# Kernel tuning notes

Hardware: AMD Instinct MI355X
Metric: run time of the kernel (lower is better)

The kernel has to match this reference:

```python
import jax, jax.numpy as jnp
import numpy as np

L_MAX = 3
N = 16384
K = 128
N_ITERS = 2
DEG = [2 * l + 1 for l in range(L_MAX + 1)]  # [1,3,5,7]


def _cg_mask():
    # zero outside selection-rule-valid (l1,l2,l) triangles and valid m ranges
    m = np.zeros((4, 4, 4, 7, 7, 7), np.float32)
    for l1 in range(L_MAX + 1):
        for l2 in range(L_MAX + 1):
            for l in range(L_MAX + 1):
                if abs(l1 - l2) <= l <= l1 + l2:
                    m[l1, l2, l, : 2 * l1 + 1, : 2 * l2 + 1, : 2 * l + 1] = 1.0
    return m


def setup_inputs() -> dict:
    key = jax.random.key(0)
    ks = jax.random.split(key, 8)
    feats = {
        f"f{l}": jax.random.normal(ks[l], (N, DEG[l], K), dtype=jnp.float32)
        for l in range(L_MAX + 1)
    }
    mixer_w = jax.random.normal(ks[4], (N_ITERS + 1, L_MAX + 1, K, K), dtype=jnp.float32) / np.sqrt(K)
    iter_w = jax.random.normal(ks[5], (N_ITERS, L_MAX + 1, K, K), dtype=jnp.float32) / np.sqrt(K)
    cg = jax.random.normal(ks[6], (4, 4, 4, 7, 7, 7), dtype=jnp.float32) * jnp.asarray(_cg_mask())
    return {**feats, "mixer_w": mixer_w, "iter_w": iter_w, "cg": cg}


def _linear(feats, w):
    # per-l channel mixing (bias-free, equivariance-preserving)
    return [jnp.einsum("nmk,kq->nmq", f, w[l]) for l, f in enumerate(feats)]


def _tensor_product(a, b, cg):
    # CG tensor product: out_l[n,m,k] = sum_{l1,l2 valid} sum_{m1,m2} cg[m1,m2,m] a_l1[n,m1,k] b_l2[n,m2,k]
    out = []
    n = a[0].shape[0]
    for l in range(L_MAX + 1):
        acc = jnp.zeros((n, DEG[l], K), dtype=a[0].dtype)
        for l1 in range(L_MAX + 1):
            for l2 in range(L_MAX + 1):
                if abs(l1 - l2) <= l <= l1 + l2:
                    c = cg[l1, l2, l, : DEG[l1], : DEG[l2], : DEG[l]]
                    acc = acc + jnp.einsum("ijm,nik,njk->nmk", c, a[l1], b[l2])
        out.append(acc)
    return out


def reference(f0, f1, f2, f3, mixer_w, iter_w, cg):
    density = [f0, f1, f2, f3]
    mixed = [_linear(density, mixer_w[i]) for i in range(N_ITERS + 1)]
    current = mixed[0]
    for t in range(N_ITERS):
        # CGIteration: tensor_product -> linear -> residual add
        tp = _tensor_product(current, mixed[t + 1], cg)
        tp = _linear(tp, iter_w[t])
        current = [c + p for c, p in zip(current, tp)]
    return tuple(current)
```

## Files before the change

kernel.cpp:

```cpp
#include <hip/hip_runtime.h>
#include <stdint.h>


#define N_ROWS 16384
#define NK (16384 * 128)

typedef float f32x4 __attribute__((ext_vector_type(4)));
typedef short short8 __attribute__((ext_vector_type(8)));
typedef __bf16 bf16x8 __attribute__((ext_vector_type(8)));

__device__ __forceinline__ uint16_t f2b(float f) {
  uint32_t u = __builtin_bit_cast(uint32_t, f);
  u += 0x7FFFu + ((u >> 16) & 1u);
  return (uint16_t)(u >> 16);
}
__device__ __forceinline__ float b2f(uint16_t h) {
  uint32_t u = ((uint32_t)h) << 16;
  return __builtin_bit_cast(float, u);
}
__device__ __forceinline__ f32x4 mfma_bf16(short8 a, short8 b, f32x4 c) {
  return __builtin_amdgcn_mfma_f32_16x16x32_bf16(
      __builtin_bit_cast(bf16x8, a), __builtin_bit_cast(bf16x8, b), c, 0, 0, 0);
}

__device__ __forceinline__ void tile_decode(int T, int& l, int& row0) {
  l = (T >= 1024) + (T >= 4096) + (T >= 9216);
  row0 = (T - l * l * 1024) * 16;
}
__device__ __forceinline__ int l_of_m(int m) { return (m > 0) + (m > 3) + (m > 8); }

__global__ __launch_bounds__(256) void k0_prep(
    const float* __restrict__ mixw, const float* __restrict__ iterw,
    const float* __restrict__ cg,
    uint16_t* __restrict__ wtmix, uint16_t* __restrict__ wtiter,
    uint16_t* __restrict__ ccat) {
  int idx = blockIdx.x * 256 + threadIdx.x;
  const int NMIX = 3 * 4 * 16384, NITR = 2 * 4 * 16384;
  if (idx < NMIX) {
    int il = idx >> 14, rem = idx & 16383, q = rem >> 7, k = rem & 127;
    wtmix[idx] = f2b(mixw[il * 16384 + k * 128 + q]);
  } else if (idx < NMIX + NITR) {
    int o = idx - NMIX;
    int tl = o >> 14, rem = o & 16383, q = rem >> 7, k = rem & 127;
    wtiter[o] = f2b(iterw[tl * 16384 + k * 128 + q]);
  } else if (idx < NMIX + NITR + 4096) {
    int o = idx - NMIX - NITR;
    int mg = o >> 8, ij = o & 255, ig = ij >> 4, jg = ij & 15;
    int l = l_of_m(mg), m = mg - l * l;
    int l1 = l_of_m(ig), i = ig - l1 * l1;
    int l2 = l_of_m(jg), j = jg - l2 * l2;
    ccat[o] = f2b(cg[(l1 * 16 + l2 * 4 + l) * 343 + i * 49 + j * 7 + m]);
  }
}

__global__ __launch_bounds__(256) void k1_mix(
    const float* __restrict__ f0, const float* __restrict__ f1,
    const float* __restrict__ f2, const float* __restrict__ f3,
    const uint16_t* __restrict__ wtmix,
    float* __restrict__ out0, uint16_t* __restrict__ m1,
    uint16_t* __restrict__ m2) {
  int lane = threadIdx.x & 63, wid = threadIdx.x >> 6;
  int g = lane >> 4, r = lane & 15;
  int T = blockIdx.x * 4 + wid;
  int l, row0; tile_decode(T, l, row0);
  const float* F = (l == 0) ? f0 : (l == 1) ? f1 : (l == 2) ? f2 : f3;

  short8 af[4];
#pragma unroll
  for (int kk = 0; kk < 4; ++kk) {
    const float* p = F + (size_t)(row0 + r) * 128 + kk * 32 + g * 8;
    f32x4 x = *(const f32x4*)p;
    f32x4 y = *(const f32x4*)(p + 4);
    short8 v;
#pragma unroll
    for (int e = 0; e < 4; ++e) { v[e] = (short)f2b(x[e]); v[4 + e] = (short)f2b(y[e]); }
    af[kk] = v;
  }
  size_t seg = (size_t)l * l * NK;
#pragma unroll
  for (int i = 0; i < 3; ++i) {
    const uint16_t* W = wtmix + (i * 4 + l) * 16384;
#pragma unroll
    for (int qt = 0; qt < 8; ++qt) {
      f32x4 acc = {0.f, 0.f, 0.f, 0.f};
#pragma unroll
      for (int kk = 0; kk < 4; ++kk) {
        short8 bfr = *(const short8*)(W + (qt * 16 + r) * 128 + kk * 32 + g * 8);
        acc = mfma_bf16(af[kk], bfr, acc);
      }
#pragma unroll
      for (int j = 0; j < 4; ++j) {
        size_t idx = seg + (size_t)(row0 + g * 4 + j) * 128 + qt * 16 + r;
        if (i == 0) out0[idx] = acc[j];
        else if (i == 1) m1[idx] = f2b(acc[j]);
        else m2[idx] = f2b(acc[j]);
      }
    }
  }
}

__global__ __launch_bounds__(256) void k2a_tp(
    const float* __restrict__ cur, const uint16_t* __restrict__ mixedb,
    const uint16_t* __restrict__ ccat, uint16_t* __restrict__ tpo) {
  __shared__ __align__(16) uint16_t lds[4][2048 + 2048 + 4096];
  int lane = threadIdx.x & 63, wid = threadIdx.x >> 6;
  int g = lane >> 4, r = lane & 15;
  int n = blockIdx.x * 4 + wid;
  uint16_t* a_s = lds[wid];
  uint16_t* b_s = a_s + 2048;
  uint16_t* pt  = b_s + 2048;

#pragma unroll
  for (int m = 0; m < 16; ++m) {
    int l = l_of_m(m), loc = m - l * l;
    size_t base = (size_t)l * l * NK + ((size_t)n * (2 * l + 1) + loc) * 128;
    a_s[m * 128 + lane]      = f2b(cur[base + lane]);
    a_s[m * 128 + 64 + lane] = f2b(cur[base + 64 + lane]);
    ((unsigned int*)(b_s + m * 128))[lane] = ((const unsigned int*)(mixedb + base))[lane];
  }
  __syncthreads();

  short8 cf[8];
#pragma unroll
  for (int cc = 0; cc < 8; ++cc)
    cf[cc] = *(const short8*)(ccat + r * 256 + cc * 32 + g * 8);

  f32x4 acc[8];
#pragma unroll
  for (int kt = 0; kt < 8; ++kt) acc[kt] = f32x4{0.f, 0.f, 0.f, 0.f};

  const int jb = (g & 1) * 8;
#pragma unroll
  for (int cc = 0; cc < 8; ++cc) {
    int iG = cc * 2 + (g >> 1);
#pragma unroll
    for (int ki = 0; ki < 8; ++ki) {
      int k = ki * 16 + r;
      float av = b2f(a_s[iG * 128 + k]);
      short8 pv;
#pragma unroll
      for (int e = 0; e < 8; ++e) {
        float bv = b2f(b_s[(jb + e) * 128 + k]);
        pv[e] = (short)f2b(av * bv);
      }
      *(short8*)((char*)pt + (((k * 64) + g * 16) ^ ((k & 3) << 4))) = pv;
    }
    __syncthreads();
#pragma unroll
    for (int kt = 0; kt < 8; ++kt) {
      int k = kt * 16 + r;
      short8 pb = *(const short8*)((char*)pt + (((k * 64) + g * 16) ^ ((k & 3) << 4)));
      acc[kt] = mfma_bf16(cf[cc], pb, acc[kt]);
    }
    __syncthreads();
  }

#pragma unroll
  for (int kt = 0; kt < 8; ++kt) {
#pragma unroll
    for (int j = 0; j < 4; ++j) {
      int m = g * 4 + j;
      int l = l_of_m(m), loc = m - l * l;
      size_t idx = (size_t)l * l * NK + ((size_t)n * (2 * l + 1) + loc) * 128 + kt * 16 + r;
      tpo[idx] = f2b(acc[kt][j]);
    }
  }
}

__global__ __launch_bounds__(256) void k2b_lin(
    const uint16_t* __restrict__ tp, const uint16_t* __restrict__ wt,
    float* __restrict__ cur) {
  int lane = threadIdx.x & 63, wid = threadIdx.x >> 6;
  int g = lane >> 4, r = lane & 15;
  int T = blockIdx.x * 4 + wid;
  int l, row0; tile_decode(T, l, row0);
  size_t seg = (size_t)l * l * NK;

  short8 af[4];
#pragma unroll
  for (int kk = 0; kk < 4; ++kk)
    af[kk] = *(const short8*)(tp + seg + (size_t)(row0 + r) * 128 + kk * 32 + g * 8);

  const uint16_t* W = wt + l * 16384;
#pragma unroll
  for (int qt = 0; qt < 8; ++qt) {
    f32x4 acc = {0.f, 0.f, 0.f, 0.f};
#pragma unroll
    for (int kk = 0; kk < 4; ++kk) {
      short8 b = *(const short8*)(W + (qt * 16 + r) * 128 + kk * 32 + g * 8);
      acc = mfma_bf16(af[kk], b, acc);
    }
#pragma unroll
    for (int j = 0; j < 4; ++j) {
      size_t idx = seg + (size_t)(row0 + g * 4 + j) * 128 + qt * 16 + r;
      cur[idx] += acc[j];
    }
  }
}

extern "C" void kernel_launch(void* const* d_in, const int* in_sizes, int n_in,
                              void* d_out, int out_size, void* d_ws, size_t ws_size,
                              hipStream_t stream) {
  const float* f0    = (const float*)d_in[0];
  const float* f1    = (const float*)d_in[1];
  const float* f2    = (const float*)d_in[2];
  const float* f3    = (const float*)d_in[3];
  const float* mixw  = (const float*)d_in[4];
  const float* iterw = (const float*)d_in[5];
  const float* cg    = (const float*)d_in[6];
  float* out = (float*)d_out;

  uint16_t* wtmix  = (uint16_t*)d_ws;
  uint16_t* wtiter = wtmix + 196608;
  uint16_t* ccat   = wtiter + 131072;
  uint16_t* m1     = ccat + 4096;
  uint16_t* m2     = m1 + 33554432;
  uint16_t* tpb    = m2 + 33554432;

  k0_prep<<<1296, 256, 0, stream>>>(mixw, iterw, cg, wtmix, wtiter, ccat);
  k1_mix<<<4096, 256, 0, stream>>>(f0, f1, f2, f3, wtmix, out, m1, m2);
  k2a_tp<<<4096, 256, 0, stream>>>(out, m1, ccat, tpb);
  k2b_lin<<<4096, 256, 0, stream>>>(tpb, wtiter + 0 * 4 * 16384, out);
  k2a_tp<<<4096, 256, 0, stream>>>(out, m2, ccat, tpb);
  k2b_lin<<<4096, 256, 0, stream>>>(tpb, wtiter + 1 * 4 * 16384, out);
}
```

Before: 669.9 us.

## Fuse mixing, tensor products and iteration linears into one per-node kernel

```diff
diff --git a/kernel.cpp b/kernel.cpp
--- a/kernel.cpp
+++ b/kernel.cpp
@@ -2,12 +2,17 @@
 #include <stdint.h>
 
 
-#define N_ROWS 16384
 #define NK (16384 * 128)
 
 typedef float f32x4 __attribute__((ext_vector_type(4)));
 typedef short short8 __attribute__((ext_vector_type(8)));
 typedef __bf16 bf16x8 __attribute__((ext_vector_type(8)));
+typedef uint32_t u32x4 __attribute__((ext_vector_type(4)));
+
+typedef short8 short8a __attribute__((may_alias));
+typedef f32x4 f32x4a __attribute__((may_alias));
+typedef uint32_t u32a __attribute__((may_alias));
+typedef float floata __attribute__((may_alias));
 
 __device__ __forceinline__ uint16_t f2b(float f) {
   uint32_t u = __builtin_bit_cast(uint32_t, f);
@@ -18,14 +23,14 @@
   uint32_t u = ((uint32_t)h) << 16;
   return __builtin_bit_cast(float, u);
 }
+__device__ __forceinline__ uint32_t pk2(float lo, float hi) {
+  uint32_t r;
+  asm("v_cvt_pk_bf16_f32 %0, %1, %2" : "=v"(r) : "v"(lo), "v"(hi));
+  return r;
+}
 __device__ __forceinline__ f32x4 mfma_bf16(short8 a, short8 b, f32x4 c) {
   return __builtin_amdgcn_mfma_f32_16x16x32_bf16(
       __builtin_bit_cast(bf16x8, a), __builtin_bit_cast(bf16x8, b), c, 0, 0, 0);
-}
-
-__device__ __forceinline__ void tile_decode(int T, int& l, int& row0) {
-  l = (T >= 1024) + (T >= 4096) + (T >= 9216);
-  row0 = (T - l * l * 1024) * 16;
 }
 __device__ __forceinline__ int l_of_m(int m) { return (m > 0) + (m > 3) + (m > 8); }
 
@@ -53,149 +58,139 @@
   }
 }
 
-__global__ __launch_bounds__(256) void k1_mix(
+__global__ __launch_bounds__(256, 2) void k_fused(
     const float* __restrict__ f0, const float* __restrict__ f1,
     const float* __restrict__ f2, const float* __restrict__ f3,
-    const uint16_t* __restrict__ wtmix,
-    float* __restrict__ out0, uint16_t* __restrict__ m1,
-    uint16_t* __restrict__ m2) {
-  int lane = threadIdx.x & 63, wid = threadIdx.x >> 6;
-  int g = lane >> 4, r = lane & 15;
-  int T = blockIdx.x * 4 + wid;
-  int l, row0; tile_decode(T, l, row0);
-  const float* F = (l == 0) ? f0 : (l == 1) ? f1 : (l == 2) ? f2 : f3;
+    const uint16_t* __restrict__ wtmix, const uint16_t* __restrict__ wtiter,
+    const uint16_t* __restrict__ ccat, float* __restrict__ out) {
+  __shared__ __align__(16) uint16_t lds[4][5632];
+  const int lane = threadIdx.x & 63, wid = threadIdx.x >> 6;
+  const int g = lane >> 4, r = lane & 15;
+  const int n = blockIdx.x * 4 + wid;
+  uint16_t* const ct = lds[wid];
+  uint16_t* const bt = ct + 2560;
+
+  const int lr = l_of_m(r), locr = r - lr * lr;
+  const float* Fp = (lr == 0) ? f0 : (lr == 1) ? f1 : (lr == 2) ? f2 : f3;
+  Fp += ((size_t)n * (2 * lr + 1) + locr) * 128;
 
   short8 af[4];
 #pragma unroll
   for (int kk = 0; kk < 4; ++kk) {
-    const float* p = F + (size_t)(row0 + r) * 128 + kk * 32 + g * 8;
-    f32x4 x = *(const f32x4*)p;
-    f32x4 y = *(const f32x4*)(p + 4);
-    short8 v;
-#pragma unroll
-    for (int e = 0; e < 4; ++e) { v[e] = (short)f2b(x[e]); v[4 + e] = (short)f2b(y[e]); }
-    af[kk] = v;
-  }
-  size_t seg = (size_t)l * l * NK;
-#pragma unroll
-  for (int i = 0; i < 3; ++i) {
-    const uint16_t* W = wtmix + (i * 4 + l) * 16384;
+    f32x4 x = *(const f32x4a*)(Fp + kk * 32 + g * 8);
+    f32x4 y = *(const f32x4a*)(Fp + kk * 32 + g * 8 + 4);
+    u32x4 p = {pk2(x[0], x[1]), pk2(x[2], x[3]), pk2(y[0], y[1]), pk2(y[2], y[3])};
+    af[kk] = __builtin_bit_cast(short8, p);
+  }
+
+  auto gemm_masked = [&](f32x4 (&acc)[8], const short8 (&fr)[4],
+                         const uint16_t* Wb) {
+    const short8 z = {0, 0, 0, 0, 0, 0, 0, 0};
+    for (int lb = 0; lb < 4; ++lb) {
+      const bool on = (lr == lb);
+      short8 s0 = on ? fr[0] : z, s1 = on ? fr[1] : z;
+      short8 s2 = on ? fr[2] : z, s3 = on ? fr[3] : z;
+      const uint16_t* W = Wb + lb * 16384;
+#pragma unroll
+      for (int qt = 0; qt < 8; ++qt) {
+        const uint16_t* Wq = W + (qt * 16 + r) * 128 + g * 8;
+        acc[qt] = mfma_bf16(s0, *(const short8a*)(Wq), acc[qt]);
+        acc[qt] = mfma_bf16(s1, *(const short8a*)(Wq + 32), acc[qt]);
+        acc[qt] = mfma_bf16(s2, *(const short8a*)(Wq + 64), acc[qt]);
+        acc[qt] = mfma_bf16(s3, *(const short8a*)(Wq + 96), acc[qt]);
+      }
+    }
+  };
+
+  f32x4 cur[8], tm[8];
+  uint32_t m1p[16], m2p[16];
+#pragma unroll
+  for (int qt = 0; qt < 8; ++qt) cur[qt] = f32x4{0, 0, 0, 0};
+  gemm_masked(cur, af, wtmix);
+#pragma unroll
+  for (int qt = 0; qt < 8; ++qt) tm[qt] = f32x4{0, 0, 0, 0};
+  gemm_masked(tm, af, wtmix + 4 * 16384);
+#pragma unroll
+  for (int qt = 0; qt < 8; ++qt) {
+    m1p[qt * 2] = pk2(tm[qt][0], tm[qt][1]);
+    m1p[qt * 2 + 1] = pk2(tm[qt][2], tm[qt][3]);
+  }
+#pragma unroll
+  for (int qt = 0; qt < 8; ++qt) tm[qt] = f32x4{0, 0, 0, 0};
+  gemm_masked(tm, af, wtmix + 8 * 16384);
+#pragma unroll
+  for (int qt = 0; qt < 8; ++qt) {
+    m2p[qt * 2] = pk2(tm[qt][0], tm[qt][1]);
+    m2p[qt * 2 + 1] = pk2(tm[qt][2], tm[qt][3]);
+  }
+
+  const int jb = (g & 1) * 8, ih = g >> 1;
+
+  auto iter = [&](const uint32_t (&mp)[16], const uint16_t* Wit) {
 #pragma unroll
     for (int qt = 0; qt < 8; ++qt) {
-      f32x4 acc = {0.f, 0.f, 0.f, 0.f};
-#pragma unroll
-      for (int kk = 0; kk < 4; ++kk) {
-        short8 bfr = *(const short8*)(W + (qt * 16 + r) * 128 + kk * 32 + g * 8);
-        acc = mfma_bf16(af[kk], bfr, acc);
+      const int k = qt * 16 + r;
+      *(u32a*)&ct[k * 20 + g * 4] = pk2(cur[qt][0], cur[qt][1]);
+      *(u32a*)&ct[k * 20 + g * 4 + 2] = pk2(cur[qt][2], cur[qt][3]);
+      *(u32a*)&bt[k * 24 + g * 4] = mp[qt * 2];
+      *(u32a*)&bt[k * 24 + g * 4 + 2] = mp[qt * 2 + 1];
+    }
+    f32x4 acc[8];
+#pragma unroll
+    for (int ki = 0; ki < 8; ++ki) acc[ki] = f32x4{0, 0, 0, 0};
+    for (int cc = 0; cc < 8; ++cc) {
+      const short8 cfr = *(const short8a*)(ccat + r * 256 + cc * 32 + g * 8);
+#pragma unroll
+      for (int ki = 0; ki < 8; ++ki) {
+        const int k = ki * 16 + r;
+        short8 bw = *(const short8a*)&bt[k * 24 + jb];
+        u32x4 bu = __builtin_bit_cast(u32x4, bw);
+        const float av = b2f(ct[k * 20 + cc * 2 + ih]);
+        float bf0 = __builtin_bit_cast(float, bu[0] << 16);
+        float bf1 = __builtin_bit_cast(float, bu[0] & 0xffff0000u);
+        float bf2 = __builtin_bit_cast(float, bu[1] << 16);
+        float bf3 = __builtin_bit_cast(float, bu[1] & 0xffff0000u);
+        float bf4 = __builtin_bit_cast(float, bu[2] << 16);
+        float bf5 = __builtin_bit_cast(float, bu[2] & 0xffff0000u);
+        float bf6 = __builtin_bit_cast(float, bu[3] << 16);
+        float bf7 = __builtin_bit_cast(float, bu[3] & 0xffff0000u);
+        u32x4 pu = {pk2(av * bf0, av * bf1), pk2(av * bf2, av * bf3),
+                    pk2(av * bf4, av * bf5), pk2(av * bf6, av * bf7)};
+        acc[ki] = mfma_bf16(cfr, __builtin_bit_cast(short8, pu), acc[ki]);
       }
+    }
+#pragma unroll
+    for (int ki = 0; ki < 8; ++ki) {
+      const int k = ki * 16 + r;
 #pragma unroll
       for (int j = 0; j < 4; ++j) {
-        size_t idx = seg + (size_t)(row0 + g * 4 + j) * 128 + qt * 16 + r;
-        if (i == 0) out0[idx] = acc[j];
-        else if (i == 1) m1[idx] = f2b(acc[j]);
-        else m2[idx] = f2b(acc[j]);
+        const int m = g * 4 + j;
+        ct[m * 128 + (k ^ ((m & 12) << 2))] = (uint16_t)pk2(acc[ki][j], acc[ki][j]);
       }
     }
-  }
-}
-
-__global__ __launch_bounds__(256) void k2a_tp(
-    const float* __restrict__ cur, const uint16_t* __restrict__ mixedb,
-    const uint16_t* __restrict__ ccat, uint16_t* __restrict__ tpo) {
-  __shared__ __align__(16) uint16_t lds[4][2048 + 2048 + 4096];
-  int lane = threadIdx.x & 63, wid = threadIdx.x >> 6;
-  int g = lane >> 4, r = lane & 15;
-  int n = blockIdx.x * 4 + wid;
-  uint16_t* a_s = lds[wid];
-  uint16_t* b_s = a_s + 2048;
-  uint16_t* pt  = b_s + 2048;
-
-#pragma unroll
-  for (int m = 0; m < 16; ++m) {
-    int l = l_of_m(m), loc = m - l * l;
-    size_t base = (size_t)l * l * NK + ((size_t)n * (2 * l + 1) + loc) * 128;
-    a_s[m * 128 + lane]      = f2b(cur[base + lane]);
-    a_s[m * 128 + 64 + lane] = f2b(cur[base + 64 + lane]);
-    ((unsigned int*)(b_s + m * 128))[lane] = ((const unsigned int*)(mixedb + base))[lane];
-  }
-  __syncthreads();
-
-  short8 cf[8];
-#pragma unroll
-  for (int cc = 0; cc < 8; ++cc)
-    cf[cc] = *(const short8*)(ccat + r * 256 + cc * 32 + g * 8);
-
-  f32x4 acc[8];
-#pragma unroll
-  for (int kt = 0; kt < 8; ++kt) acc[kt] = f32x4{0.f, 0.f, 0.f, 0.f};
-
-  const int jb = (g & 1) * 8;
-#pragma unroll
-  for (int cc = 0; cc < 8; ++cc) {
-    int iG = cc * 2 + (g >> 1);
-#pragma unroll
-    for (int ki = 0; ki < 8; ++ki) {
-      int k = ki * 16 + r;
-      float av = b2f(a_s[iG * 128 + k]);
-      short8 pv;
-#pragma unroll
-      for (int e = 0; e < 8; ++e) {
-        float bv = b2f(b_s[(jb + e) * 128 + k]);
-        pv[e] = (short)f2b(av * bv);
-      }
-      *(short8*)((char*)pt + (((k * 64) + g * 16) ^ ((k & 3) << 4))) = pv;
-    }
-    __syncthreads();
-#pragma unroll
-    for (int kt = 0; kt < 8; ++kt) {
-      int k = kt * 16 + r;
-      short8 pb = *(const short8*)((char*)pt + (((k * 64) + g * 16) ^ ((k & 3) << 4)));
-      acc[kt] = mfma_bf16(cf[cc], pb, acc[kt]);
-    }
-    __syncthreads();
-  }
-
-#pragma unroll
-  for (int kt = 0; kt < 8; ++kt) {
-#pragma unroll
-    for (int j = 0; j < 4; ++j) {
-      int m = g * 4 + j;
-      int l = l_of_m(m), loc = m - l * l;
-      size_t idx = (size_t)l * l * NK + ((size_t)n * (2 * l + 1) + loc) * 128 + kt * 16 + r;
-      tpo[idx] = f2b(acc[kt][j]);
-    }
-  }
-}
-
-__global__ __launch_bounds__(256) void k2b_lin(
-    const uint16_t* __restrict__ tp, const uint16_t* __restrict__ wt,
-    float* __restrict__ cur) {
-  int lane = threadIdx.x & 63, wid = threadIdx.x >> 6;
-  int g = lane >> 4, r = lane & 15;
-  int T = blockIdx.x * 4 + wid;
-  int l, row0; tile_decode(T, l, row0);
-  size_t seg = (size_t)l * l * NK;
-
-  short8 af[4];
-#pragma unroll
-  for (int kk = 0; kk < 4; ++kk)
-    af[kk] = *(const short8*)(tp + seg + (size_t)(row0 + r) * 128 + kk * 32 + g * 8);
-
-  const uint16_t* W = wt + l * 16384;
-#pragma unroll
-  for (int qt = 0; qt < 8; ++qt) {
-    f32x4 acc = {0.f, 0.f, 0.f, 0.f};
-#pragma unroll
-    for (int kk = 0; kk < 4; ++kk) {
-      short8 b = *(const short8*)(W + (qt * 16 + r) * 128 + kk * 32 + g * 8);
-      acc = mfma_bf16(af[kk], b, acc);
-    }
-#pragma unroll
-    for (int j = 0; j < 4; ++j) {
-      size_t idx = seg + (size_t)(row0 + g * 4 + j) * 128 + qt * 16 + r;
-      cur[idx] += acc[j];
-    }
-  }
+    short8 afl[4];
+#pragma unroll
+    for (int kk = 0; kk < 4; ++kk)
+      afl[kk] = *(const short8a*)&ct[r * 128 + ((kk * 32 + g * 8) ^ ((r & 12) << 2))];
+    gemm_masked(cur, afl, Wit);
+  };
+
+  iter(m1p, wtiter);
+  iter(m2p, wtiter + 4 * 16384);
+
+  floata* outs = (floata*)ct;
+#pragma unroll
+  for (int qt = 0; qt < 8; ++qt)
+#pragma unroll
+    for (int j = 0; j < 4; ++j)
+      outs[(g * 4 + j) * 132 + qt * 16 + r] = cur[qt][j];
+  const int mm = lane >> 2, c3 = lane & 3;
+  const int lo = l_of_m(mm), locm = mm - lo * lo;
+  float* op = out + (size_t)lo * lo * NK + ((size_t)n * (2 * lo + 1) + locm) * 128 + c3 * 4;
+  const floata* ip = outs + mm * 132 + c3 * 4;
+#pragma unroll
+  for (int q = 0; q < 8; ++q)
+    *(f32x4a*)(op + q * 16) = *(const f32x4a*)(ip + q * 16);
 }
 
 extern "C" void kernel_launch(void* const* d_in, const int* in_sizes, int n_in,
@@ -213,14 +208,7 @@
   uint16_t* wtmix  = (uint16_t*)d_ws;
   uint16_t* wtiter = wtmix + 196608;
   uint16_t* ccat   = wtiter + 131072;
-  uint16_t* m1     = ccat + 4096;
-  uint16_t* m2     = m1 + 33554432;
-  uint16_t* tpb    = m2 + 33554432;
 
   k0_prep<<<1296, 256, 0, stream>>>(mixw, iterw, cg, wtmix, wtiter, ccat);
-  k1_mix<<<4096, 256, 0, stream>>>(f0, f1, f2, f3, wtmix, out, m1, m2);
-  k2a_tp<<<4096, 256, 0, stream>>>(out, m1, ccat, tpb);
-  k2b_lin<<<4096, 256, 0, stream>>>(tpb, wtiter + 0 * 4 * 16384, out);
-  k2a_tp<<<4096, 256, 0, stream>>>(out, m2, ccat, tpb);
-  k2b_lin<<<4096, 256, 0, stream>>>(tpb, wtiter + 1 * 4 * 16384, out);
-}
+  k_fused<<<4096, 256, 0, stream>>>(f0, f1, f2, f3, wtmix, wtiter, ccat, out);
+}
```

Result: slower. 1.191 ms (+77.7%).
